# Kernel tuning notes

Measured on AMD Instinct MI355X. Metric: run time of the kernel, lower is better.

## Reference

```python
import jax, jax.numpy as jnp
import numpy as np

EMBED_DIM = 1024
NUM_HEADS = 8                      # diff-attn heads; effective standard heads = 2*NUM_HEADS
HEAD_DIM = EMBED_DIM // NUM_HEADS // 2   # 64
DEPTH = 12
LAMBDA_INIT = 0.8 - 0.6 * float(np.exp(-0.3 * DEPTH))
RMS_EPS = 1e-5


def _rope_interleaved(x, cos, sin):
    # x: [B,S,H,D]; cos,sin: [S,D//2]. GPT-J style: rotate (even, odd) pairs.
    x1, x2 = x[..., ::2], x[..., 1::2]
    c = cos[None, :, None, :]
    s = sin[None, :, None, :]
    o1 = x1 * c - x2 * s
    o2 = x1 * s + x2 * c
    return jnp.stack([o1, o2], axis=-1).reshape(x.shape)


def _causal_attn(q, k, v, scale):
    # q,k: [B,S,H,D]; v: [B,S,H,Dv] -> out [B,S,H,Dv]
    S = q.shape[1]
    scores = jnp.einsum('bqhd,bkhd->bhqk', q, k) * scale
    causal = jnp.tril(jnp.ones((S, S), dtype=bool))
    scores = jnp.where(causal[None, None], scores, jnp.finfo(scores.dtype).min)
    p = jax.nn.softmax(scores, axis=-1)
    return jnp.einsum('bhqk,bkhd->bqhd', p, v)


def setup_inputs() -> dict:
    key = jax.random.key(0)
    ks = jax.random.split(key, 10)
    B, S, E, D = 1, 2048, EMBED_DIM, HEAD_DIM
    x = jax.random.normal(ks[0], (B, S, E), jnp.float32)
    # real rotary tables, rotary_dim = head_dim = 64 -> cos/sin [S, 32]
    inv_freq = 1.0 / (10000.0 ** (np.arange(0, D, 2, dtype=np.float64) / D))
    freqs = np.outer(np.arange(S, dtype=np.float64), inv_freq)
    cos = jnp.asarray(np.cos(freqs), jnp.float32)
    sin = jnp.asarray(np.sin(freqs), jnp.float32)
    sc = 1.0 / np.sqrt(E)
    wq = jax.random.normal(ks[1], (E, E), jnp.float32) * sc
    wk = jax.random.normal(ks[2], (E, E), jnp.float32) * sc
    wv = jax.random.normal(ks[3], (E, E), jnp.float32) * sc
    wo = jax.random.normal(ks[4], (E, E), jnp.float32) * sc
    lambda_q1 = jax.random.normal(ks[5], (D,), jnp.float32) * 0.1
    lambda_k1 = jax.random.normal(ks[6], (D,), jnp.float32) * 0.1
    lambda_q2 = jax.random.normal(ks[7], (D,), jnp.float32) * 0.1
    lambda_k2 = jax.random.normal(ks[8], (D,), jnp.float32) * 0.1
    subln_weight = jnp.ones((2 * D,), jnp.float32)
    return dict(x=x, cos=cos, sin=sin, wq=wq, wk=wk, wv=wv, wo=wo,
                lambda_q1=lambda_q1, lambda_k1=lambda_k1,
                lambda_q2=lambda_q2, lambda_k2=lambda_k2,
                subln_weight=subln_weight)


def reference(x, cos, sin, wq, wk, wv, wo,
              lambda_q1, lambda_k1, lambda_q2, lambda_k2, subln_weight):
    B, S, E = x.shape
    H, D = NUM_HEADS, HEAD_DIM
    q = (x @ wq).reshape(B, S, 2 * H, D)
    k = (x @ wk).reshape(B, S, 2 * H, D)
    v = (x @ wv).reshape(B, S, H, 2 * D)
    q = _rope_interleaved(q, cos, sin)
    k = _rope_interleaved(k, cos, sin)
    q = q.reshape(B, S, H, 2, D)
    k = k.reshape(B, S, H, 2, D)
    q1, q2 = q[..., 0, :], q[..., 1, :]
    k1, k2 = k[..., 0, :], k[..., 1, :]
    scale = D ** -0.5  # flash_attn default softmax scale
    a1 = _causal_attn(q1, k1, v, scale)  # [B,S,H,2D]
    a2 = _causal_attn(q2, k2, v, scale)
    lam1 = jnp.exp(jnp.sum(lambda_q1 * lambda_k1))
    lam2 = jnp.exp(jnp.sum(lambda_q2 * lambda_k2))
    lam_full = lam1 - lam2 + LAMBDA_INIT
    attn = a1 - lam_full * a2
    # sublayer RMSNorm over 2*head_dim, computed in fp32
    ms = jnp.mean(jnp.square(attn.astype(jnp.float32)), axis=-1, keepdims=True)
    attn = (attn.astype(jnp.float32) * jax.lax.rsqrt(ms + RMS_EPS)).astype(attn.dtype)
    attn = attn * subln_weight
    attn = attn * (1.0 - LAMBDA_INIT)
    attn = attn.reshape(B, S, E)
    return attn @ wo
```

## Files before the change

### kernel.cpp

```cpp
#include <hip/hip_runtime.h>
#include <hip/hip_bf16.h>

#define SEQ 2048
#define EMB 1024
#define NH 8
#define HD 64
#define DVH 128
#define LAMBDA_INIT 0.7836057665316245f
#define ONE_MINUS_LI 0.2163942334683755f
#define RMS_EPS 1e-5f
#define QK_SCALE 0.18033688011112042f

typedef __attribute__((ext_vector_type(8))) short short8_t;
typedef __attribute__((ext_vector_type(4))) float f32x4;
typedef __attribute__((ext_vector_type(4))) unsigned uint4_t;

__device__ __forceinline__ short f2bf(float f) {
    __hip_bfloat16 h = __float2bfloat16(f);
    return *reinterpret_cast<short*>(&h);
}
__device__ __forceinline__ float bf2f(short s) {
    unsigned u = ((unsigned)(unsigned short)s) << 16;
    return __uint_as_float(u);
}
__device__ __forceinline__ float fast_exp2(float x) {
    float r;
    asm("v_exp_f32 %0, %1" : "=v"(r) : "v"(x));
    return r;
}
__device__ __forceinline__ void gload16(const void* g, void* l) {
    __builtin_amdgcn_global_load_lds((const __attribute__((address_space(1))) unsigned int*)g,
                                     (__attribute__((address_space(3))) unsigned int*)l, 16, 0, 0);
}
__device__ __forceinline__ short8_t rope8(short8_t v, const float* cp, const float* sp) {
    f32x4 c4 = *(const f32x4*)cp;
    f32x4 s4 = *(const f32x4*)sp;
    short8_t o;
#pragma unroll
    for (int i = 0; i < 4; i++) {
        float e = bf2f(v[2 * i]), od = bf2f(v[2 * i + 1]);
        o[2 * i] = f2bf(e * c4[i] - od * s4[i]);
        o[2 * i + 1] = f2bf(e * s4[i] + od * c4[i]);
    }
    return o;
}

__global__ __launch_bounds__(256) void k_prep(const float* __restrict__ x, short* __restrict__ xb,
                                              const float* __restrict__ w0, const float* __restrict__ w1,
                                              const float* __restrict__ w2, const float* __restrict__ w3,
                                              short* __restrict__ o0, short* __restrict__ o1,
                                              short* __restrict__ o2, short* __restrict__ o3,
                                              const float* __restrict__ lq1, const float* __restrict__ lk1,
                                              const float* __restrict__ lq2, const float* __restrict__ lk2,
                                              float* __restrict__ lam) {
    const int bid = blockIdx.x;
    const int tid = threadIdx.x;
    if (bid < 2048) {
        int i = bid * 256 + tid;
        const float4* xv = (const float4*)x;
        float4 v = xv[i];
        short4 r = make_short4(f2bf(v.x), f2bf(v.y), f2bf(v.z), f2bf(v.w));
        *(short4*)(xb + i * 4) = r;
    } else if (bid < 3072) {
        int t = bid - 2048;
        int bz = t >> 8, by = (t >> 4) & 15, bx = t & 15;
        const float* w = bz == 0 ? w0 : bz == 1 ? w1 : bz == 2 ? w2 : w3;
        short* o = bz == 0 ? o0 : bz == 1 ? o1 : bz == 2 ? o2 : o3;
        __shared__ float tbuf[64][65];
        int r0 = by * 64, c0 = bx * 64;
        int col = tid & 63, rb = tid >> 6;
#pragma unroll
        for (int i = 0; i < 16; i++) {
            int row = rb + i * 4;
            tbuf[row][col] = w[(r0 + row) * EMB + c0 + col];
        }
        __syncthreads();
#pragma unroll
        for (int i = 0; i < 16; i++) {
            int fr = rb + i * 4;
            o[(c0 + fr) * EMB + r0 + col] = f2bf(tbuf[col][fr]);
        }
    } else {
        if (tid < 64) {
            float p1 = lq1[tid] * lk1[tid], p2 = lq2[tid] * lk2[tid];
#pragma unroll
            for (int off = 32; off >= 1; off >>= 1) {
                p1 += __shfl_xor(p1, off);
                p2 += __shfl_xor(p2, off);
            }
            if (tid == 0) lam[0] = expf(p1) - expf(p2) + LAMBDA_INIT;
        }
    }
}

template <int MI, int NI, int OUTM>
__global__ __launch_bounds__(256) void k_gemm(const short* __restrict__ A,
                                              const short* __restrict__ B0,
                                              const short* __restrict__ B1,
                                              const short* __restrict__ B2,
                                              short* __restrict__ Cq, short* __restrict__ Ck,
                                              short* __restrict__ Cv, float* __restrict__ Cf) {
    constexpr int BM = MI * 32, BN = NI * 32, BK = 64;
    __shared__ short Abuf[BM * BK];
    __shared__ short Bbuf[BN * BK];
    const int bn = blockIdx.x * BN;
    const int bm = blockIdx.y * BM;
    const int nsel = bn >> 10;
    const int nloc = bn & 1023;
    const short* Bt = nsel == 0 ? B0 : (nsel == 1 ? B1 : B2);
    const int tid = threadIdx.x;
    const int w = tid >> 6, l = tid & 63;
    const int lr = l & 15, lg = l >> 4;
    const int wm = (w >> 1) * (MI * 16), wn = (w & 1) * (NI * 16);
    const int lrow8 = l >> 3, lchunk = l & 7;
    const int schunk = (lchunk ^ lrow8) * 8;

    f32x4 acc[MI][NI];
#pragma unroll
    for (int mi = 0; mi < MI; mi++)
#pragma unroll
        for (int ni = 0; ni < NI; ni++) acc[mi][ni] = f32x4{0.f, 0.f, 0.f, 0.f};

    for (int k0 = 0; k0 < EMB; k0 += BK) {
#pragma unroll
        for (int j = 0; j < BM / 32; j++) {
            int r0 = w * (BM / 4) + j * 8;
            gload16(A + (size_t)(bm + r0 + lrow8) * EMB + k0 + schunk, &Abuf[r0 * BK]);
        }
#pragma unroll
        for (int j = 0; j < BN / 32; j++) {
            int r0 = w * (BN / 4) + j * 8;
            gload16(Bt + (size_t)(nloc + r0 + lrow8) * EMB + k0 + schunk, &Bbuf[r0 * BK]);
        }
        __syncthreads();
#pragma unroll
        for (int kk = 0; kk < 2; kk++) {
            const int pcs = (((kk << 2) + lg) ^ (lr & 7)) << 3;
            short8_t af[MI], bf[NI];
#pragma unroll
            for (int mi = 0; mi < MI; mi++)
                af[mi] = *(const short8_t*)&Abuf[(wm + mi * 16 + lr) * BK + pcs];
#pragma unroll
            for (int ni = 0; ni < NI; ni++)
                bf[ni] = *(const short8_t*)&Bbuf[(wn + ni * 16 + lr) * BK + pcs];
#pragma unroll
            for (int mi = 0; mi < MI; mi++)
#pragma unroll
                for (int ni = 0; ni < NI; ni++)
                    acc[mi][ni] =
                        __builtin_amdgcn_mfma_f32_16x16x32_bf16(af[mi], bf[ni], acc[mi][ni], 0, 0, 0);
        }
        __syncthreads();
    }
#pragma unroll
    for (int mi = 0; mi < MI; mi++)
#pragma unroll
        for (int ni = 0; ni < NI; ni++)
#pragma unroll
            for (int r = 0; r < 4; r++) {
                int row = bm + wm + mi * 16 + lg * 4 + r;
                int col = wn + ni * 16 + lr;
                if (OUTM == 0) {
                    if (nsel < 2) {
                        int ci = nloc + col;
                        int hh = ci >> 7, c = ci & 127;
                        (nsel == 0 ? Cq : Ck)[(hh << 18) + row * 128 + c] = f2bf(acc[mi][ni][r]);
                    } else {
                        Cv[row * EMB + nloc + col] = f2bf(acc[mi][ni][r]);
                    }
                } else {
                    Cf[row * EMB + bn + col] = acc[mi][ni][r];
                }
            }
}

__global__ __launch_bounds__(256) void k_tile_kv(const short* __restrict__ Kh,
                                                 const short* __restrict__ Vb,
                                                 const float* __restrict__ cosT,
                                                 const float* __restrict__ sinT,
                                                 short* __restrict__ Ktl,
                                                 short* __restrict__ Vtl) {
    const int kb = blockIdx.x, h = blockIdx.y;
    const int k0 = kb * 32;
    const int t = threadIdx.x;
    __shared__ short VS[32][130];
    {
        const int r = t >> 3, c0 = (t & 7) * 16;
        const short* src = Vb + (size_t)(k0 + r) * EMB + h * 128 + c0;
        *(short8_t*)&VS[r][c0] = *(const short8_t*)(src);
        *(short8_t*)&VS[r][c0 + 8] = *(const short8_t*)(src + 8);
    }
    {
        const short* kh = Kh + ((size_t)h << 18);
#pragma unroll
        for (int it = 0; it < 2; it++) {
            int idx = t + it * 256;
            int row = idx >> 4, c = idx & 15;
            short8_t v = *(const short8_t*)(kh + (size_t)(k0 + row) * 128 + c * 8);
            const size_t cs = (size_t)(k0 + row) * 32 + (c & 7) * 4;
            v = rope8(v, cosT + cs, sinT + cs);
            int comp = c >> 3, s = (c >> 2) & 1, lg = c & 3;
            int tt = row >> 4, lq = row & 15;
            int lane = lg * 16 + lq;
            *(short8_t*)(Ktl + ((size_t)(h * 64 + kb) * 8 + comp * 4 + tt * 2 + s) * 512 + lane * 8) = v;
        }
    }
    __syncthreads();
#pragma unroll
    for (int it = 0; it < 2; it++) {
        int idx = t + it * 256;
        int dt = idx >> 6, l = idx & 63;
        int lq = l & 15, lg = l >> 4;
        short8_t v;
#pragma unroll
        for (int j = 0; j < 8; j++) v[j] = VS[(j >> 2) * 16 + lg * 4 + (j & 3)][dt * 16 + lq];
        *(short8_t*)(Vtl + ((size_t)(h * 64 + kb) * 8 + dt) * 512 + l * 8) = v;
    }
}

__global__ __launch_bounds__(512) void k_attn(const short* __restrict__ Qh,
                                              const short* __restrict__ Ktl,
                                              const short* __restrict__ Vtl,
                                              const float* __restrict__ cosT,
                                              const float* __restrict__ sinT,
                                              const float* __restrict__ lamp,
                                              const float* __restrict__ subln,
                                              short* __restrict__ Ab) {
    const int bid = blockIdx.x;
    const int h = bid & 7;
    const int tile = 63 - (bid >> 3);
    const int q0 = tile * 32;
    const int tid = threadIdx.x;
    const int w = tid >> 6, l = tid & 63;
    const int lq = l & 15, lg = l >> 4;
    const int comp = w >> 2, ks = w & 3;

    __shared__ __align__(16) float buf[2][2][16][132];
    __shared__ float LBp[2][4][16];

    const int nb = tile + 1;

    short8_t qf0[2], qf1[2];
    {
        const short* qp = Qh + ((size_t)h << 18) + (size_t)(q0 + lq) * 128 + (comp << 6) + lg * 8;
        const size_t s0 = (size_t)(q0 + lq) * 32, s1 = (size_t)(q0 + 16 + lq) * 32;
        qf0[0] = rope8(*(const short8_t*)(qp), cosT + s0 + lg * 4, sinT + s0 + lg * 4);
        qf0[1] = rope8(*(const short8_t*)(qp + 32), cosT + s0 + 16 + lg * 4, sinT + s0 + 16 + lg * 4);
        qf1[0] = rope8(*(const short8_t*)(qp + 16 * 128), cosT + s1 + lg * 4, sinT + s1 + lg * 4);
        qf1[1] = rope8(*(const short8_t*)(qp + 16 * 128 + 32), cosT + s1 + 16 + lg * 4,
                       sinT + s1 + 16 + lg * 4);
    }
    f32x4 zero4 = {0.f, 0.f, 0.f, 0.f};
    f32x4 o0[8], o1[8];
#pragma unroll
    for (int dt = 0; dt < 8; dt++) {
        o0[dt] = zero4;
        o1[dt] = zero4;
    }
    float ls0 = 0.f, ls1 = 0.f;

    for (int kb = ks; kb < nb; kb += 4) {
        const int k0 = kb * 32;
        const short* vtb = Vtl + (size_t)(h * 64 + kb) * 4096 + l * 8;
        const short* ktb = Ktl + ((size_t)(h * 64 + kb) * 8 + comp * 4) * 512 + l * 8;
        short8_t vf[8];
#pragma unroll
        for (int dt = 0; dt < 8; dt++) vf[dt] = *(const short8_t*)(vtb + dt * 512);
        short8_t kf[2][2];
#pragma unroll
        for (int tt = 0; tt < 2; tt++) {
            kf[tt][0] = *(const short8_t*)(ktb + (tt * 2) * 512);
            kf[tt][1] = *(const short8_t*)(ktb + (tt * 2 + 1) * 512);
        }
        f32x4 s0[2], s1[2];
#pragma unroll
        for (int tt = 0; tt < 2; tt++) {
            s0[tt] = zero4;
            s0[tt] = __builtin_amdgcn_mfma_f32_16x16x32_bf16(kf[tt][0], qf0[0], s0[tt], 0, 0, 0);
            s0[tt] = __builtin_amdgcn_mfma_f32_16x16x32_bf16(kf[tt][1], qf0[1], s0[tt], 0, 0, 0);
            s1[tt] = zero4;
            s1[tt] = __builtin_amdgcn_mfma_f32_16x16x32_bf16(kf[tt][0], qf1[0], s1[tt], 0, 0, 0);
            s1[tt] = __builtin_amdgcn_mfma_f32_16x16x32_bf16(kf[tt][1], qf1[1], s1[tt], 0, 0, 0);
        }
        float p0[8], p1[8];
#pragma unroll
        for (int tt = 0; tt < 2; tt++)
#pragma unroll
            for (int r = 0; r < 4; r++) {
                p0[tt * 4 + r] = s0[tt][r] * QK_SCALE;
                p1[tt * 4 + r] = s1[tt][r] * QK_SCALE;
            }
        if (k0 + 31 > q0) {
#pragma unroll
            for (int tt = 0; tt < 2; tt++)
#pragma unroll
                for (int r = 0; r < 4; r++) {
                    int kk = k0 + tt * 16 + lg * 4 + r;
                    if (kk > q0 + lq) p0[tt * 4 + r] = -1e30f;
                    if (kk > q0 + 16 + lq) p1[tt * 4 + r] = -1e30f;
                }
        }
#pragma unroll
        for (int i = 0; i < 8; i++) {
            p0[i] = fast_exp2(p0[i]);
            ls0 += p0[i];
            p1[i] = fast_exp2(p1[i]);
            ls1 += p1[i];
        }
        uint4_t pu0, pu1;
#pragma unroll
        for (int pr = 0; pr < 4; pr++) {
            float2 f0 = {p0[2 * pr], p0[2 * pr + 1]};
            float2 f1 = {p1[2 * pr], p1[2 * pr + 1]};
            __hip_bfloat162 h0 = __float22bfloat162_rn(f0);
            __hip_bfloat162 h1 = __float22bfloat162_rn(f1);
            unsigned u0, u1;
            __builtin_memcpy(&u0, &h0, 4);
            __builtin_memcpy(&u1, &h1, 4);
            pu0[pr] = u0;
            pu1[pr] = u1;
        }
        short8_t pa0, pa1;
        __builtin_memcpy(&pa0, &pu0, 16);
        __builtin_memcpy(&pa1, &pu1, 16);
#pragma unroll
        for (int dt = 0; dt < 8; dt++) {
            o0[dt] = __builtin_amdgcn_mfma_f32_16x16x32_bf16(pa0, vf[dt], o0[dt], 0, 0, 0);
            o1[dt] = __builtin_amdgcn_mfma_f32_16x16x32_bf16(pa1, vf[dt], o1[dt], 0, 0, 0);
        }
    }

    ls0 += __shfl_xor(ls0, 16);
    ls0 += __shfl_xor(ls0, 32);
    ls1 += __shfl_xor(ls1, 16);
    ls1 += __shfl_xor(ls1, 32);

#pragma unroll 1
    for (int sub = 0; sub < 2; sub++) {
        const f32x4* o = sub ? o1 : o0;
        const float lsum = sub ? ls1 : ls0;
        const int qbase = q0 + sub * 16;
        if (sub) __syncthreads();
        if (ks >= 2) {
#pragma unroll
            for (int dt = 0; dt < 8; dt++)
#pragma unroll
                for (int r = 0; r < 4; r++) buf[comp][ks - 2][lg * 4 + r][dt * 16 + lq] = o[dt][r];
            if (l < 16) LBp[comp][ks][l] = lsum;
        }
        __syncthreads();
        f32x4 oacc[8];
        float lacc = lsum;
        if (ks < 2) {
#pragma unroll
            for (int dt = 0; dt < 8; dt++)
#pragma unroll
                for (int r = 0; r < 4; r++)
                    oacc[dt][r] = o[dt][r] + buf[comp][ks][lg * 4 + r][dt * 16 + lq];
            lacc = lsum + LBp[comp][ks + 2][lq];
        }
        __syncthreads();
        if (ks == 1) {
#pragma unroll
            for (int dt = 0; dt < 8; dt++)
#pragma unroll
                for (int r = 0; r < 4; r++) buf[comp][0][lg * 4 + r][dt * 16 + lq] = oacc[dt][r];
            if (l < 16) LBp[comp][1][l] = lacc;
        }
        __syncthreads();
        if (ks == 0) {
#pragma unroll
            for (int dt = 0; dt < 8; dt++)
#pragma unroll
                for (int r = 0; r < 4; r++) oacc[dt][r] += buf[comp][0][lg * 4 + r][dt * 16 + lq];
            lacc += LBp[comp][1][lq];
            const float cs = comp ? lamp[0] : 1.f;
            float inv[4];
#pragma unroll
            for (int r = 0; r < 4; r++) inv[r] = cs / __shfl(lacc, lg * 4 + r);
#pragma unroll
            for (int dt = 0; dt < 8; dt++)
#pragma unroll
                for (int r = 0; r < 4; r++)
                    buf[comp][1][lg * 4 + r][dt * 16 + lq] = oacc[dt][r] * inv[r];
        }
        __syncthreads();
        if (tid < 128) {
            const int row = tid >> 3;
            const int c0 = (tid & 7) * 16;
            float a[16], ss = 0.f;
#pragma unroll
            for (int j = 0; j < 16; j++) {
                a[j] = buf[0][1][row][c0 + j] - buf[1][1][row][c0 + j];
                ss += a[j] * a[j];
            }
            ss += __shfl_xor(ss, 1);
            ss += __shfl_xor(ss, 2);
            ss += __shfl_xor(ss, 4);
            const float sc = rsqrtf(ss * (1.0f / 128.0f) + RMS_EPS) * ONE_MINUS_LI;
            short8_t r8;
#pragma unroll
            for (int j = 0; j < 8; j++) r8[j] = f2bf(a[j] * sc * subln[c0 + j]);
            *(short8_t*)(Ab + (size_t)(qbase + row) * EMB + h * DVH + c0) = r8;
#pragma unroll
            for (int j = 0; j < 8; j++) r8[j] = f2bf(a[8 + j] * sc * subln[c0 + 8 + j]);
            *(short8_t*)(Ab + (size_t)(qbase + row) * EMB + h * DVH + c0 + 8) = r8;
        }
    }
}

extern "C" void kernel_launch(void* const* d_in, const int* in_sizes, int n_in,
                              void* d_out, int out_size, void* d_ws, size_t ws_size,
                              hipStream_t stream) {
    const float* x = (const float*)d_in[0];
    const float* cosT = (const float*)d_in[1];
    const float* sinT = (const float*)d_in[2];
    const float* wq = (const float*)d_in[3];
    const float* wk = (const float*)d_in[4];
    const float* wv = (const float*)d_in[5];
    const float* wo = (const float*)d_in[6];
    const float* lq1 = (const float*)d_in[7];
    const float* lk1 = (const float*)d_in[8];
    const float* lq2 = (const float*)d_in[9];
    const float* lk2 = (const float*)d_in[10];
    const float* subln = (const float*)d_in[11];
    float* out = (float*)d_out;
    char* ws = (char*)d_ws;
    const size_t MB = 1 << 20;
    short* xb = (short*)(ws);
    short* Vtl = (short*)(ws);
    short* wqt = (short*)(ws + 4 * MB);
    short* wkt = (short*)(ws + 6 * MB);
    short* wvt = (short*)(ws + 8 * MB);
    short* wot = (short*)(ws + 10 * MB);
    short* Qh = (short*)(ws + 12 * MB);
    short* Kh = (short*)(ws + 16 * MB);
    short* Vb = (short*)(ws + 20 * MB);
    short* Ktl = (short*)(ws + 24 * MB);
    short* Ab = (short*)(ws + 28 * MB);
    float* lam = (float*)(ws + 32 * MB);

    k_prep<<<3073, 256, 0, stream>>>(x, xb, wq, wk, wv, wo, wqt, wkt, wvt, wot, lq1, lk1, lq2,
                                     lk2, lam);
    k_gemm<2, 4, 0><<<dim3(24, 32), 256, 0, stream>>>(xb, wqt, wkt, wvt, Qh, Kh, Vb, nullptr);
    k_tile_kv<<<dim3(64, 8), 256, 0, stream>>>(Kh, Vb, cosT, sinT, Ktl, Vtl);
    k_attn<<<512, 512, 0, stream>>>(Qh, Ktl, Vtl, cosT, sinT, lam, subln, Ab);
    k_gemm<2, 4, 1><<<dim3(8, 32), 256, 0, stream>>>(Ab, wot, wot, wot, nullptr, nullptr, nullptr, out);
}
```

Before: 87.39 us.

## Fuse RoPE and K/V tiling into QKV GEMM epilogue; double-buffer KV loads in attention

The QKV GEMM epilogue now applies RoPE to Q and K using lane shuffles. It also writes K and V directly into the MFMA-tiled layouts through a shared-memory staging tile, which removes the separate k_tile_kv kernel and the RoPE work on Q inside attention. The attention loop is restructured into two-way register double buffering of K/V fragments so the next block's loads overlap compute, and launch bounds request 2 blocks per CU. This costs extra registers and a more complex GEMM epilogue with scattered cos/sin loads.

```diff
diff --git a/kernel.cpp b/kernel.cpp
--- a/kernel.cpp
+++ b/kernel.cpp
@@ -13,7 +13,6 @@
 
 typedef __attribute__((ext_vector_type(8))) short short8_t;
 typedef __attribute__((ext_vector_type(4))) float f32x4;
-typedef __attribute__((ext_vector_type(4))) unsigned uint4_t;
 
 __device__ __forceinline__ short f2bf(float f) {
     __hip_bfloat16 h = __float2bfloat16(f);
@@ -31,18 +30,6 @@
 __device__ __forceinline__ void gload16(const void* g, void* l) {
     __builtin_amdgcn_global_load_lds((const __attribute__((address_space(1))) unsigned int*)g,
                                      (__attribute__((address_space(3))) unsigned int*)l, 16, 0, 0);
-}
-__device__ __forceinline__ short8_t rope8(short8_t v, const float* cp, const float* sp) {
-    f32x4 c4 = *(const f32x4*)cp;
-    f32x4 s4 = *(const f32x4*)sp;
-    short8_t o;
-#pragma unroll
-    for (int i = 0; i < 4; i++) {
-        float e = bf2f(v[2 * i]), od = bf2f(v[2 * i + 1]);
-        o[2 * i] = f2bf(e * c4[i] - od * s4[i]);
-        o[2 * i + 1] = f2bf(e * s4[i] + od * c4[i]);
-    }
-    return o;
 }
 
 __global__ __launch_bounds__(256) void k_prep(const float* __restrict__ x, short* __restrict__ xb,
@@ -98,11 +85,14 @@
                                               const short* __restrict__ B0,
                                               const short* __restrict__ B1,
                                               const short* __restrict__ B2,
-                                              short* __restrict__ Cq, short* __restrict__ Ck,
-                                              short* __restrict__ Cv, float* __restrict__ Cf) {
+                                              const float* __restrict__ cosT,
+                                              const float* __restrict__ sinT,
+                                              short* __restrict__ Cq, short* __restrict__ Ktl,
+                                              short* __restrict__ Vtl, float* __restrict__ Cf) {
     constexpr int BM = MI * 32, BN = NI * 32, BK = 64;
-    __shared__ short Abuf[BM * BK];
-    __shared__ short Bbuf[BN * BK];
+    __shared__ short SH[BM * BK + BN * BK];
+    short* Abuf = SH;
+    short* Bbuf = SH + BM * BK;
     const int bn = blockIdx.x * BN;
     const int bm = blockIdx.y * BM;
     const int nsel = bn >> 10;
@@ -152,80 +142,95 @@
         }
         __syncthreads();
     }
-#pragma unroll
-    for (int mi = 0; mi < MI; mi++)
-#pragma unroll
-        for (int ni = 0; ni < NI; ni++)
-#pragma unroll
-            for (int r = 0; r < 4; r++) {
-                int row = bm + wm + mi * 16 + lg * 4 + r;
-                int col = wn + ni * 16 + lr;
-                if (OUTM == 0) {
-                    if (nsel < 2) {
-                        int ci = nloc + col;
-                        int hh = ci >> 7, c = ci & 127;
-                        (nsel == 0 ? Cq : Ck)[(hh << 18) + row * 128 + c] = f2bf(acc[mi][ni][r]);
-                    } else {
-                        Cv[row * EMB + nloc + col] = f2bf(acc[mi][ni][r]);
-                    }
-                } else {
+
+    if (OUTM == 1) {
+#pragma unroll
+        for (int mi = 0; mi < MI; mi++)
+#pragma unroll
+            for (int ni = 0; ni < NI; ni++)
+#pragma unroll
+                for (int r = 0; r < 4; r++) {
+                    int row = bm + wm + mi * 16 + lg * 4 + r;
+                    int col = wn + ni * 16 + lr;
                     Cf[row * EMB + bn + col] = acc[mi][ni][r];
                 }
+        return;
+    }
+    const int hh = nloc >> 7;
+    if (nsel < 2) {
+        short* tile = SH;
+#pragma unroll
+        for (int mi = 0; mi < MI; mi++)
+#pragma unroll
+            for (int ni = 0; ni < NI; ni++) {
+                const int c = wn + ni * 16 + lr;
+                const int p = (c & 63) >> 1;
+#pragma unroll
+                for (int r = 0; r < 4; r++) {
+                    const int row = wm + mi * 16 + lg * 4 + r;
+                    const int grow = bm + row;
+                    float v = acc[mi][ni][r];
+                    float partner = __shfl_xor(v, 1);
+                    float cs = cosT[grow * 32 + p], sn = sinT[grow * 32 + p];
+                    float out = (lr & 1) ? (partner * sn + v * cs) : (v * cs - partner * sn);
+                    if (nsel == 0)
+                        Cq[((size_t)hh << 18) + (size_t)grow * 128 + c] = f2bf(out);
+                    else
+                        tile[row * 136 + c] = f2bf(out);
+                }
             }
-}
-
-__global__ __launch_bounds__(256) void k_tile_kv(const short* __restrict__ Kh,
-                                                 const short* __restrict__ Vb,
-                                                 const float* __restrict__ cosT,
-                                                 const float* __restrict__ sinT,
-                                                 short* __restrict__ Ktl,
-                                                 short* __restrict__ Vtl) {
-    const int kb = blockIdx.x, h = blockIdx.y;
-    const int k0 = kb * 32;
-    const int t = threadIdx.x;
-    __shared__ short VS[32][130];
-    {
-        const int r = t >> 3, c0 = (t & 7) * 16;
-        const short* src = Vb + (size_t)(k0 + r) * EMB + h * 128 + c0;
-        *(short8_t*)&VS[r][c0] = *(const short8_t*)(src);
-        *(short8_t*)&VS[r][c0 + 8] = *(const short8_t*)(src + 8);
-    }
-    {
-        const short* kh = Kh + ((size_t)h << 18);
-#pragma unroll
-        for (int it = 0; it < 2; it++) {
-            int idx = t + it * 256;
-            int row = idx >> 4, c = idx & 15;
-            short8_t v = *(const short8_t*)(kh + (size_t)(k0 + row) * 128 + c * 8);
-            const size_t cs = (size_t)(k0 + row) * 32 + (c & 7) * 4;
-            v = rope8(v, cosT + cs, sinT + cs);
-            int comp = c >> 3, s = (c >> 2) & 1, lg = c & 3;
-            int tt = row >> 4, lq = row & 15;
-            int lane = lg * 16 + lq;
-            *(short8_t*)(Ktl + ((size_t)(h * 64 + kb) * 8 + comp * 4 + tt * 2 + s) * 512 + lane * 8) = v;
-        }
-    }
-    __syncthreads();
-#pragma unroll
-    for (int it = 0; it < 2; it++) {
-        int idx = t + it * 256;
-        int dt = idx >> 6, l = idx & 63;
-        int lq = l & 15, lg = l >> 4;
-        short8_t v;
-#pragma unroll
-        for (int j = 0; j < 8; j++) v[j] = VS[(j >> 2) * 16 + lg * 4 + (j & 3)][dt * 16 + lq];
-        *(short8_t*)(Vtl + ((size_t)(h * 64 + kb) * 8 + dt) * 512 + l * 8) = v;
-    }
-}
-
-__global__ __launch_bounds__(512) void k_attn(const short* __restrict__ Qh,
-                                              const short* __restrict__ Ktl,
-                                              const short* __restrict__ Vtl,
-                                              const float* __restrict__ cosT,
-                                              const float* __restrict__ sinT,
-                                              const float* __restrict__ lamp,
-                                              const float* __restrict__ subln,
-                                              short* __restrict__ Ab) {
+        if (nsel == 1) {
+            __syncthreads();
+            const int kb0 = blockIdx.y * 2;
+#pragma unroll
+            for (int i = 0; i < 4; i++) {
+                int flat = tid + i * 256;
+                int kbi = flat >> 9, rest = flat & 511;
+                int slot = rest >> 6, ln = rest & 63;
+                int comp = slot >> 2, tt = (slot >> 1) & 1, s = slot & 1;
+                int lgg = ln >> 4, lqq = ln & 15;
+                int row = kbi * 32 + tt * 16 + lqq;
+                int fb = comp * 64 + s * 32 + lgg * 8;
+                short8_t v = *(const short8_t*)&tile[row * 136 + fb];
+                *(short8_t*)(Ktl + ((size_t)(hh * 64 + kb0 + kbi) * 8 + slot) * 512 + ln * 8) = v;
+            }
+        }
+    } else {
+        short* tile = SH;
+#pragma unroll
+        for (int mi = 0; mi < MI; mi++)
+#pragma unroll
+            for (int ni = 0; ni < NI; ni++) {
+                const int c = wn + ni * 16 + lr;
+#pragma unroll
+                for (int r = 0; r < 4; r++) {
+                    const int row = wm + mi * 16 + lg * 4 + r;
+                    tile[row * 136 + c] = f2bf(acc[mi][ni][r]);
+                }
+            }
+        __syncthreads();
+        const int kb0 = blockIdx.y * 2;
+#pragma unroll
+        for (int i = 0; i < 4; i++) {
+            int flat = tid + i * 256;
+            int kbi = flat >> 9, rest = flat & 511;
+            int dt = rest >> 6, ln = rest & 63;
+            int lgg = ln >> 4, lqq = ln & 15;
+            short8_t v;
+#pragma unroll
+            for (int j = 0; j < 8; j++)
+                v[j] = tile[(kbi * 32 + 16 * (j >> 2) + 4 * lgg + (j & 3)) * 136 + dt * 16 + lqq];
+            *(short8_t*)(Vtl + ((size_t)(hh * 64 + kb0 + kbi) * 8 + dt) * 512 + ln * 8) = v;
+        }
+    }
+}
+
+__global__ __launch_bounds__(512, 2) void k_attn(const short* __restrict__ Qh,
+                                                 const short* __restrict__ Ktl,
+                                                 const short* __restrict__ Vtl,
+                                                 const float* __restrict__ lamp,
+                                                 const float* __restrict__ subln,
+                                                 short* __restrict__ Ab) {
     const int bid = blockIdx.x;
     const int h = bid & 7;
     const int tile = 63 - (bid >> 3);
@@ -243,12 +248,10 @@
     short8_t qf0[2], qf1[2];
     {
         const short* qp = Qh + ((size_t)h << 18) + (size_t)(q0 + lq) * 128 + (comp << 6) + lg * 8;
-        const size_t s0 = (size_t)(q0 + lq) * 32, s1 = (size_t)(q0 + 16 + lq) * 32;
-        qf0[0] = rope8(*(const short8_t*)(qp), cosT + s0 + lg * 4, sinT + s0 + lg * 4);
-        qf0[1] = rope8(*(const short8_t*)(qp + 32), cosT + s0 + 16 + lg * 4, sinT + s0 + 16 + lg * 4);
-        qf1[0] = rope8(*(const short8_t*)(qp + 16 * 128), cosT + s1 + lg * 4, sinT + s1 + lg * 4);
-        qf1[1] = rope8(*(const short8_t*)(qp + 16 * 128 + 32), cosT + s1 + 16 + lg * 4,
-                       sinT + s1 + 16 + lg * 4);
+        qf0[0] = *(const short8_t*)(qp);
+        qf0[1] = *(const short8_t*)(qp + 32);
+        qf1[0] = *(const short8_t*)(qp + 16 * 128);
+        qf1[1] = *(const short8_t*)(qp + 16 * 128 + 32);
     }
     f32x4 zero4 = {0.f, 0.f, 0.f, 0.f};
     f32x4 o0[8], o1[8];
@@ -259,76 +262,83 @@
     }
     float ls0 = 0.f, ls1 = 0.f;
 
-    for (int kb = ks; kb < nb; kb += 4) {
-        const int k0 = kb * 32;
-        const short* vtb = Vtl + (size_t)(h * 64 + kb) * 4096 + l * 8;
-        const short* ktb = Ktl + ((size_t)(h * 64 + kb) * 8 + comp * 4) * 512 + l * 8;
-        short8_t vf[8];
-#pragma unroll
-        for (int dt = 0; dt < 8; dt++) vf[dt] = *(const short8_t*)(vtb + dt * 512);
-        short8_t kf[2][2];
-#pragma unroll
-        for (int tt = 0; tt < 2; tt++) {
-            kf[tt][0] = *(const short8_t*)(ktb + (tt * 2) * 512);
-            kf[tt][1] = *(const short8_t*)(ktb + (tt * 2 + 1) * 512);
-        }
-        f32x4 s0[2], s1[2];
-#pragma unroll
-        for (int tt = 0; tt < 2; tt++) {
-            s0[tt] = zero4;
-            s0[tt] = __builtin_amdgcn_mfma_f32_16x16x32_bf16(kf[tt][0], qf0[0], s0[tt], 0, 0, 0);
-            s0[tt] = __builtin_amdgcn_mfma_f32_16x16x32_bf16(kf[tt][1], qf0[1], s0[tt], 0, 0, 0);
-            s1[tt] = zero4;
-            s1[tt] = __builtin_amdgcn_mfma_f32_16x16x32_bf16(kf[tt][0], qf1[0], s1[tt], 0, 0, 0);
-            s1[tt] = __builtin_amdgcn_mfma_f32_16x16x32_bf16(kf[tt][1], qf1[1], s1[tt], 0, 0, 0);
-        }
-        float p0[8], p1[8];
-#pragma unroll
-        for (int tt = 0; tt < 2; tt++)
-#pragma unroll
-            for (int r = 0; r < 4; r++) {
-                p0[tt * 4 + r] = s0[tt][r] * QK_SCALE;
-                p1[tt * 4 + r] = s1[tt][r] * QK_SCALE;
-            }
-        if (k0 + 31 > q0) {
-#pragma unroll
-            for (int tt = 0; tt < 2; tt++)
-#pragma unroll
-                for (int r = 0; r < 4; r++) {
-                    int kk = k0 + tt * 16 + lg * 4 + r;
-                    if (kk > q0 + lq) p0[tt * 4 + r] = -1e30f;
-                    if (kk > q0 + 16 + lq) p1[tt * 4 + r] = -1e30f;
-                }
-        }
-#pragma unroll
-        for (int i = 0; i < 8; i++) {
-            p0[i] = fast_exp2(p0[i]);
-            ls0 += p0[i];
-            p1[i] = fast_exp2(p1[i]);
-            ls1 += p1[i];
-        }
-        uint4_t pu0, pu1;
-#pragma unroll
-        for (int pr = 0; pr < 4; pr++) {
-            float2 f0 = {p0[2 * pr], p0[2 * pr + 1]};
-            float2 f1 = {p1[2 * pr], p1[2 * pr + 1]};
-            __hip_bfloat162 h0 = __float22bfloat162_rn(f0);
-            __hip_bfloat162 h1 = __float22bfloat162_rn(f1);
-            unsigned u0, u1;
-            __builtin_memcpy(&u0, &h0, 4);
-            __builtin_memcpy(&u1, &h1, 4);
-            pu0[pr] = u0;
-            pu1[pr] = u1;
-        }
-        short8_t pa0, pa1;
-        __builtin_memcpy(&pa0, &pu0, 16);
-        __builtin_memcpy(&pa1, &pu1, 16);
-#pragma unroll
-        for (int dt = 0; dt < 8; dt++) {
-            o0[dt] = __builtin_amdgcn_mfma_f32_16x16x32_bf16(pa0, vf[dt], o0[dt], 0, 0, 0);
-            o1[dt] = __builtin_amdgcn_mfma_f32_16x16x32_bf16(pa1, vf[dt], o1[dt], 0, 0, 0);
-        }
-    }
+    short8_t vfA[8], vfB[8];
+    short8_t kfA[2][2], kfB[2][2];
+
+#define LOADKV(VF, KF, KB)                                                                  \
+    {                                                                                       \
+        const short* vtb = Vtl + (size_t)(h * 64 + (KB)) * 4096 + l * 8;                    \
+        const short* ktb = Ktl + ((size_t)(h * 64 + (KB)) * 8 + comp * 4) * 512 + l * 8;    \
+        _Pragma("unroll") for (int dt = 0; dt < 8; dt++) VF[dt] =                           \
+            *(const short8_t*)(vtb + dt * 512);                                             \
+        _Pragma("unroll") for (int tt = 0; tt < 2; tt++) {                                  \
+            KF[tt][0] = *(const short8_t*)(ktb + (tt * 2) * 512);                           \
+            KF[tt][1] = *(const short8_t*)(ktb + (tt * 2 + 1) * 512);                       \
+        }                                                                                   \
+    }
+
+#define PROC(VF, KF, KB)                                                                     \
+    {                                                                                        \
+        const int k0p = (KB) * 32;                                                          \
+        f32x4 s0[2], s1[2];                                                                  \
+        _Pragma("unroll") for (int tt = 0; tt < 2; tt++) {                                   \
+            s0[tt] = zero4;                                                                  \
+            s0[tt] = __builtin_amdgcn_mfma_f32_16x16x32_bf16(KF[tt][0], qf0[0], s0[tt], 0, 0, 0); \
+            s0[tt] = __builtin_amdgcn_mfma_f32_16x16x32_bf16(KF[tt][1], qf0[1], s0[tt], 0, 0, 0); \
+            s1[tt] = zero4;                                                                  \
+            s1[tt] = __builtin_amdgcn_mfma_f32_16x16x32_bf16(KF[tt][0], qf1[0], s1[tt], 0, 0, 0); \
+            s1[tt] = __builtin_amdgcn_mfma_f32_16x16x32_bf16(KF[tt][1], qf1[1], s1[tt], 0, 0, 0); \
+        }                                                                                    \
+        float p0[8], p1[8];                                                                  \
+        _Pragma("unroll") for (int tt = 0; tt < 2; tt++)                                     \
+            _Pragma("unroll") for (int r = 0; r < 4; r++) {                                  \
+                p0[tt * 4 + r] = s0[tt][r] * QK_SCALE;                                       \
+                p1[tt * 4 + r] = s1[tt][r] * QK_SCALE;                                       \
+            }                                                                                \
+        if (k0p + 31 > q0) {                                                                 \
+            _Pragma("unroll") for (int tt = 0; tt < 2; tt++)                                 \
+                _Pragma("unroll") for (int r = 0; r < 4; r++) {                              \
+                    int kk = k0p + tt * 16 + lg * 4 + r;                                     \
+                    if (kk > q0 + lq) p0[tt * 4 + r] = -1e30f;                               \
+                    if (kk > q0 + 16 + lq) p1[tt * 4 + r] = -1e30f;                          \
+                }                                                                            \
+        }                                                                                    \
+        _Pragma("unroll") for (int i = 0; i < 8; i++) {                                      \
+            p0[i] = fast_exp2(p0[i]);                                                        \
+            ls0 += p0[i];                                                                    \
+            p1[i] = fast_exp2(p1[i]);                                                        \
+            ls1 += p1[i];                                                                    \
+        }                                                                                    \
+        unsigned pu0[4], pu1[4];                                                             \
+        _Pragma("unroll") for (int pr = 0; pr < 4; pr++) {                                   \
+            float2 f0 = {p0[2 * pr], p0[2 * pr + 1]};                                        \
+            float2 f1 = {p1[2 * pr], p1[2 * pr + 1]};                                        \
+            __hip_bfloat162 h0 = __float22bfloat162_rn(f0);                                  \
+            __hip_bfloat162 h1 = __float22bfloat162_rn(f1);                                  \
+            __builtin_memcpy(&pu0[pr], &h0, 4);                                              \
+            __builtin_memcpy(&pu1[pr], &h1, 4);                                              \
+        }                                                                                    \
+        short8_t pa0, pa1;                                                                   \
+        __builtin_memcpy(&pa0, pu0, 16);                                                     \
+        __builtin_memcpy(&pa1, pu1, 16);                                                     \
+        _Pragma("unroll") for (int dt = 0; dt < 8; dt++) {                                   \
+            o0[dt] = __builtin_amdgcn_mfma_f32_16x16x32_bf16(pa0, VF[dt], o0[dt], 0, 0, 0);  \
+            o1[dt] = __builtin_amdgcn_mfma_f32_16x16x32_bf16(pa1, VF[dt], o1[dt], 0, 0, 0);  \
+        }                                                                                    \
+    }
+
+    if (ks < nb) LOADKV(vfA, kfA, ks);
+    for (int kb = ks; kb < nb; kb += 8) {
+        const bool hb = (kb + 4) < nb;
+        if (hb) LOADKV(vfB, kfB, kb + 4);
+        PROC(vfA, kfA, kb);
+        if (hb) {
+            if (kb + 8 < nb) LOADKV(vfA, kfA, kb + 8);
+            PROC(vfB, kfB, kb + 4);
+        }
+    }
+#undef LOADKV
+#undef PROC
 
     ls0 += __shfl_xor(ls0, 16);
     ls0 += __shfl_xor(ls0, 32);
@@ -428,22 +438,21 @@
     char* ws = (char*)d_ws;
     const size_t MB = 1 << 20;
     short* xb = (short*)(ws);
-    short* Vtl = (short*)(ws);
     short* wqt = (short*)(ws + 4 * MB);
     short* wkt = (short*)(ws + 6 * MB);
     short* wvt = (short*)(ws + 8 * MB);
     short* wot = (short*)(ws + 10 * MB);
     short* Qh = (short*)(ws + 12 * MB);
-    short* Kh = (short*)(ws + 16 * MB);
-    short* Vb = (short*)(ws + 20 * MB);
+    short* Vtl = (short*)(ws + 20 * MB);
     short* Ktl = (short*)(ws + 24 * MB);
     short* Ab = (short*)(ws + 28 * MB);
     float* lam = (float*)(ws + 32 * MB);
 
     k_prep<<<3073, 256, 0, stream>>>(x, xb, wq, wk, wv, wo, wqt, wkt, wvt, wot, lq1, lk1, lq2,
                                      lk2, lam);
-    k_gemm<2, 4, 0><<<dim3(24, 32), 256, 0, stream>>>(xb, wqt, wkt, wvt, Qh, Kh, Vb, nullptr);
-    k_tile_kv<<<dim3(64, 8), 256, 0, stream>>>(Kh, Vb, cosT, sinT, Ktl, Vtl);
-    k_attn<<<512, 512, 0, stream>>>(Qh, Ktl, Vtl, cosT, sinT, lam, subln, Ab);
-    k_gemm<2, 4, 1><<<dim3(8, 32), 256, 0, stream>>>(Ab, wot, wot, wot, nullptr, nullptr, nullptr, out);
-}
+    k_gemm<2, 4, 0><<<dim3(24, 32), 256, 0, stream>>>(xb, wqt, wkt, wvt, cosT, sinT, Qh, Ktl,
+                                                      Vtl, nullptr);
+    k_attn<<<512, 512, 0, stream>>>(Qh, Ktl, Vtl, lam, subln, Ab);
+    k_gemm<2, 4, 1><<<dim3(8, 32), 256, 0, stream>>>(Ab, wot, wot, wot, nullptr, nullptr,
+                                                     nullptr, nullptr, nullptr, out);
+}
```

Result: faster. 83.33 us (-4.7%).
